# Kernel tuning notes

Hardware: AMD Instinct MI355X
Metric: run time of the kernel (lower is better)

## Reference

```python
import jax, jax.numpy as jnp
import numpy as np

H = 512; V = 100; V1 = V + 1; T = 20; L = 2; B = 1024; M = 5; K = 10; DFF = 4 * H
NEG = -1e9


def _ln(x, g, b):
    m = x.mean(-1, keepdims=True)
    v = x.var(-1, keepdims=True)
    return (x - m) / jnp.sqrt(v + 1e-5) * g + b


def _attn(q_in, kv_in, iw, ib, ow, ob, mask):
    # single-head attention, inputs [T,B,H] / [S,B,H]
    q = q_in @ iw[:H].T + ib[:H]
    k = kv_in @ iw[H:2 * H].T + ib[H:2 * H]
    v = kv_in @ iw[2 * H:].T + ib[2 * H:]
    s = jnp.einsum('qbh,kbh->bqk', q, k) / jnp.sqrt(jnp.float32(H))
    if mask is not None:
        s = s + mask
    a = jax.nn.softmax(s, axis=-1)
    o = jnp.einsum('bqk,kbh->qbh', a, v)
    return o @ ow.T + ob


def _pos_encoding(max_len, d):
    pos = jnp.arange(max_len, dtype=jnp.float32)[:, None]
    div = jnp.exp(jnp.arange(0, d, 2, dtype=jnp.float32) * (-np.log(10000.0) / d))
    pe = jnp.zeros((max_len, d), jnp.float32)
    pe = pe.at[:, 0::2].set(jnp.sin(pos * div)).at[:, 1::2].set(jnp.cos(pos * div))
    return pe[:, None, :]  # [T,1,H]


def setup_inputs() -> dict:
    key = jax.random.key(0)
    ks = jax.random.split(key, 20)
    s = 0.05
    rn = lambda k, shape: jax.random.normal(k, shape, jnp.float32) * s
    return dict(
        meanings=jax.random.randint(ks[0], (B, M), 0, K),
        emb_table=rn(ks[1], (M * K, H)),
        v2e_w=rn(ks[2], (H, V1)), v2e_b=rn(ks[3], (H,)),
        e2v_w=rn(ks[4], (V1, H)), e2v_b=rn(ks[5], (V1,)),
        sa_in_w=rn(ks[6], (L, 3 * H, H)), sa_in_b=rn(ks[7], (L, 3 * H)),
        sa_out_w=rn(ks[8], (L, H, H)), sa_out_b=rn(ks[9], (L, H)),
        ca_in_w=rn(ks[10], (L, 3 * H, H)), ca_in_b=rn(ks[11], (L, 3 * H)),
        ca_out_w=rn(ks[12], (L, H, H)), ca_out_b=rn(ks[13], (L, H)),
        ff1_w=rn(ks[14], (L, DFF, H)), ff1_b=rn(ks[15], (L, DFF)),
        ff2_w=rn(ks[16], (L, H, DFF)), ff2_b=rn(ks[17], (L, H)),
        ln_g=jnp.ones((L, 3, H), jnp.float32),
        ln_b=jnp.zeros((L, 3, H), jnp.float32),
    )


def reference(meanings, emb_table, v2e_w, v2e_b, e2v_w, e2v_b,
              sa_in_w, sa_in_b, sa_out_w, sa_out_b,
              ca_in_w, ca_in_b, ca_out_w, ca_out_b,
              ff1_w, ff1_b, ff2_w, ff2_b, ln_g, ln_b):
    bsz = meanings.shape[0]
    # meanings_offset = (cumsum(ones)-1)*K == arange(M)*K
    idx = meanings + jnp.arange(M) * K          # [B,M]
    src = emb_table[idx].sum(axis=1)[None]      # [1,B,H] memory
    pe = _pos_encoding(T, H)
    # start token one-hot probabilities
    probs = jnp.zeros((1, bsz, V1), jnp.float32).at[:, :, V].set(1.0)
    outs = []
    for i in range(T):
        x = probs @ v2e_w.T + v2e_b + pe[:i + 1]            # [i+1,B,H]
        mask = jnp.triu(jnp.full((i + 1, i + 1), NEG, jnp.float32), k=1)
        for l in range(L):
            x = _ln(x + _attn(x, x, sa_in_w[l], sa_in_b[l], sa_out_w[l], sa_out_b[l], mask),
                    ln_g[l, 0], ln_b[l, 0])
            x = _ln(x + _attn(x, src, ca_in_w[l], ca_in_b[l], ca_out_w[l], ca_out_b[l], None),
                    ln_g[l, 1], ln_b[l, 1])
            ff = jax.nn.relu(x @ ff1_w[l].T + ff1_b[l]) @ ff2_w[l].T + ff2_b[l]
            x = _ln(x + ff, ln_g[l, 2], ln_b[l, 2])
        logits = x @ e2v_w.T + e2v_b                        # [i+1,B,V1]
        last = logits[-1]                                   # [B,V1]
        outs.append(last)
        probs = jnp.concatenate([probs, jax.nn.softmax(last, axis=-1)[None]], axis=0)
    return jnp.stack(outs, axis=0)                          # [T,B,V1]
```

## Files before the change

### kernel.cpp

```cpp
#include <hip/hip_runtime.h>
#include <hip/hip_bf16.h>
#include <math.h>

#define Hdim 512
#define Vv   100
#define V1n  101
#define Tt   20
#define Ln   2
#define Bb   1024
#define Mm   5
#define Kk   10
#define DFFn 2048

typedef _Float16 f16;
typedef __attribute__((ext_vector_type(8))) _Float16 f16x8;
typedef __attribute__((ext_vector_type(16))) float f32x16;

static const size_t BH  = (size_t)Bb * Hdim;
static const size_t PSP = (size_t)Bb * 128;

__device__ __forceinline__ void split2(float v, f16* s) {
    f16 h0 = (f16)v;
    float r = v - (float)h0;
    s[0] = h0; s[1] = (f16)r;
}
__device__ __forceinline__ void xsp_write(f16* __restrict__ xsp, int row, int h, float v)
{
    f16 s[2]; split2(v, s);
    size_t o = (size_t)(h >> 3) * 8192 + (size_t)row * 8 + (h & 7);
    xsp[o] = s[0]; xsp[BH + o] = s[1];
}

template<int EPI>
__global__ __launch_bounds__(256, 2) void gemm_sp(
    const f16* __restrict__ Asp, const f16* __restrict__ Wsp,
    const float* __restrict__ bias,
    float* __restrict__ C, f16* __restrict__ Csp, size_t cplane,
    int N, int Kd, int kcount, int posn)
{
    __shared__ f16 lds[16384];
    const int tid = threadIdx.x;
    const int lane = tid & 63, w = tid >> 6;
    const int wm = w >> 1, wn = w & 1;
    const int bm = blockIdx.y * 128, bn = blockIdx.x * 128;
    const int kc0 = blockIdx.z * (kcount >> 3);
    const int nt = kcount >> 5;
    const int K8 = Kd >> 3;

    size_t gA[4], gB[4]; int lA[4], lB[4];
#pragma unroll
    for (int q = 0; q < 4; ++q) {
        int cid = q * 256 + tid, slab = cid >> 7, win = cid & 127;
        int p = slab >> 2, kcr = slab & 3;
        gA[q] = ((size_t)p * K8 + kc0 + kcr) * 8192 + (size_t)bm * 8 + win * 8;
        lA[q] = slab * 1024 + win * 8;
        gB[q] = ((size_t)p * K8 + kc0 + kcr) * ((size_t)N * 8) + (size_t)bn * 8 + win * 8;
        lB[q] = 8192 + slab * 1024 + win * 8;
    }

    f32x16 acc[2][2];
#pragma unroll
    for (int mi = 0; mi < 2; ++mi)
#pragma unroll
        for (int ni = 0; ni < 2; ++ni)
#pragma unroll
            for (int j = 0; j < 16; ++j) acc[mi][ni][j] = 0.f;

    f16x8 rA[4], rB[4];
#pragma unroll
    for (int q = 0; q < 4; ++q) {
        rA[q] = *(const f16x8*)(Asp + gA[q]);
        rB[q] = *(const f16x8*)(Wsp + gB[q]);
    }

    for (int t = 0; t < nt; ++t) {
        __syncthreads();
#pragma unroll
        for (int q = 0; q < 4; ++q) {
            *(f16x8*)&lds[lA[q]] = rA[q];
            *(f16x8*)&lds[lB[q]] = rB[q];
        }
        __syncthreads();
        if (t + 1 < nt) {
#pragma unroll
            for (int q = 0; q < 4; ++q) {
                rA[q] = *(const f16x8*)(Asp + gA[q] + (size_t)(t + 1) * 32768);
                rB[q] = *(const f16x8*)(Wsp + gB[q] + (size_t)(t + 1) * 32 * N);
            }
        }
#pragma unroll
        for (int ks = 0; ks < 2; ++ks) {
            const int kb = (2 * ks + (lane >> 5)) * 1024 + (lane & 31) * 8;
            f16x8 a[2][2], b[2][2];
#pragma unroll
            for (int mi = 0; mi < 2; ++mi)
#pragma unroll
                for (int p = 0; p < 2; ++p)
                    a[mi][p] = *(const f16x8*)&lds[p * 4096 + kb + (64 * wm + 32 * mi) * 8];
#pragma unroll
            for (int ni = 0; ni < 2; ++ni)
#pragma unroll
                for (int p = 0; p < 2; ++p)
                    b[ni][p] = *(const f16x8*)&lds[8192 + p * 4096 + kb + (64 * wn + 32 * ni) * 8];
#pragma unroll
            for (int mi = 0; mi < 2; ++mi)
#pragma unroll
                for (int ni = 0; ni < 2; ++ni) {
                    f32x16 v = acc[mi][ni];
                    v = __builtin_amdgcn_mfma_f32_32x32x16_f16(a[mi][1], b[ni][0], v, 0, 0, 0);
                    v = __builtin_amdgcn_mfma_f32_32x32x16_f16(a[mi][0], b[ni][1], v, 0, 0, 0);
                    v = __builtin_amdgcn_mfma_f32_32x32x16_f16(a[mi][0], b[ni][0], v, 0, 0, 0);
                    acc[mi][ni] = v;
                }
        }
    }

    const int er0 = bm + 64 * wm + 4 * (lane >> 5);
    const int ec0 = bn + 64 * wn + (lane & 31);
#pragma unroll
    for (int mi = 0; mi < 2; ++mi) {
#pragma unroll
        for (int ni = 0; ni < 2; ++ni) {
            int col = ec0 + 32 * ni;
#pragma unroll
            for (int r = 0; r < 16; ++r) {
                int row = er0 + 32 * mi + (r & 3) + 8 * (r >> 2);
                float v = acc[mi][ni][r];
                if (EPI == 0) {
                    C[(size_t)blockIdx.z * Bb * N + (size_t)row * N + col] = v;
                } else if (EPI == 1) {
                    v = fmaxf(v + bias[col], 0.f);
                    f16 s[2]; split2(v, s);
                    size_t o = (size_t)(col >> 3) * 8192 + (size_t)row * 8 + (col & 7);
                    Csp[o] = s[0]; Csp[cplane + o] = s[1];
                } else if (EPI == 3) {
                    v += bias[col];
                    f16 s[2]; split2(v, s);
                    size_t o = (size_t)(col >> 3) * 8192 + (size_t)row * 8 + (col & 7);
                    Csp[o] = s[0]; Csp[cplane + o] = s[1];
                } else if (EPI == 4) {
                    C[(size_t)row * N + col] = v + bias[col];
                } else if (EPI == 5) {
                    v += bias[col];
                    int j2 = col & ~1;
                    float div = expf(-(float)j2 * (logf(10000.f) / (float)Hdim));
                    float ang = (float)posn * div;
                    v += (col & 1) ? cosf(ang) : sinf(ang);
                    C[(size_t)row * Hdim + col] = v;
                    f16 s[2]; split2(v, s);
                    size_t o = (size_t)(col >> 3) * 8192 + (size_t)row * 8 + (col & 7);
                    Csp[o] = s[0]; Csp[cplane + o] = s[1];
                }
            }
        }
    }
}

__global__ void split_mat(const float* __restrict__ src, f16* __restrict__ dst,
                          int Nreal, int Npad, int Kreal, int kpl)
{
    int i = blockIdx.x * 256 + threadIdx.x;
    int Kpad = 1 << kpl;
    if (i >= (Npad << kpl)) return;
    int n = i >> kpl, k = i & (Kpad - 1);
    float v = (n < Nreal && k < Kreal) ? src[(size_t)n * Kreal + k] : 0.f;
    f16 s[2]; split2(v, s);
    size_t plane = (size_t)Npad << kpl;
    size_t o = (size_t)(k >> 3) * ((size_t)Npad * 8) + (size_t)n * 8 + (k & 7);
    dst[o] = s[0]; dst[plane + o] = s[1];
}

__global__ void src_kernel(const int* __restrict__ meanings,
                           const float* __restrict__ emb, f16* __restrict__ ssp)
{
    int idx = blockIdx.x * 256 + threadIdx.x;
    int b = idx >> 9, h = idx & 511;
    float s = 0.f;
#pragma unroll
    for (int m = 0; m < Mm; ++m) {
        int row = meanings[b * Mm + m] + m * Kk;
        s += emb[(size_t)row * Hdim + h];
    }
    xsp_write(ssp, b, h, s);
}

__global__ void init_x(const float* __restrict__ v2e_w, const float* __restrict__ v2e_b,
                       float* __restrict__ x, f16* __restrict__ xsp)
{
    int idx = blockIdx.x * 256 + threadIdx.x;
    int b = idx >> 9, h = idx & 511;
    float s = v2e_w[(size_t)h * V1n + Vv] + v2e_b[h] + ((h & 1) ? 1.f : 0.f);
    x[idx] = s;
    xsp_write(xsp, b, h, s);
}

__global__ __launch_bounds__(256) void attn_fused(
    const float* __restrict__ P, const float* __restrict__ bias3h,
    float* __restrict__ kc, float* __restrict__ vc,
    f16* __restrict__ osplit, int step)
{
    __shared__ float qs[Hdim];
    __shared__ float ssm[32];
    __shared__ float wts[32];
    int b = blockIdx.x, tid = threadIdx.x, lane = tid & 63, wv = tid >> 6;
    const size_t PS = (size_t)Bb * 1536;
    const float* pb = P + (size_t)b * 1536;
#pragma unroll
    for (int c0 = 0; c0 < 2; ++c0) {
        int c = tid + c0 * 256;
        float qv = bias3h[c]        + pb[c]        + pb[PS + c];
        float kv = bias3h[512 + c]  + pb[512 + c]  + pb[PS + 512 + c];
        float vv = bias3h[1024 + c] + pb[1024 + c] + pb[PS + 1024 + c];
        qs[c] = qv;
        kc[((size_t)step * Bb + b) * Hdim + c] = kv;
        vc[((size_t)step * Bb + b) * Hdim + c] = vv;
    }
    __syncthreads();
    const float4* q4 = (const float4*)qs;
    for (int t = wv; t <= step; t += 4) {
        const float4* k4 = (const float4*)(kc + ((size_t)t * Bb + b) * Hdim);
        float4 qa = q4[lane], ka = k4[lane];
        float4 qb = q4[lane + 64], kb = k4[lane + 64];
        float p = qa.x*ka.x + qa.y*ka.y + qa.z*ka.z + qa.w*ka.w
                + qb.x*kb.x + qb.y*kb.y + qb.z*kb.z + qb.w*kb.w;
#pragma unroll
        for (int off = 32; off; off >>= 1) p += __shfl_down(p, off);
        if (!lane) ssm[t] = p * 0.044194173824159216f;
    }
    __syncthreads();
    float m = -1e30f;
    for (int t = 0; t <= step; ++t) m = fmaxf(m, ssm[t]);
    float den = 0.f;
    for (int t = 0; t <= step; ++t) den += expf(ssm[t] - m);
    if (tid <= step) wts[tid] = expf(ssm[tid] - m) / den;
    __syncthreads();
#pragma unroll
    for (int c0 = 0; c0 < 2; ++c0) {
        int h = tid + c0 * 256;
        float a2 = 0.f;
        for (int t = 0; t <= step; ++t)
            a2 += wts[t] * vc[((size_t)t * Bb + b) * Hdim + h];
        xsp_write(osplit, b, h, a2);
    }
}

__device__ __forceinline__ float2 rowstats(float v0, float v1, float* sh)
{
    __syncthreads();
    float s = v0 + v1, s2 = v0 * v0 + v1 * v1;
    int lane = threadIdx.x & 63, wv = threadIdx.x >> 6;
#pragma unroll
    for (int off = 32; off; off >>= 1) {
        s += __shfl_down(s, off);
        s2 += __shfl_down(s2, off);
    }
    if (!lane) { sh[wv] = s; sh[wv + 4] = s2; }
    __syncthreads();
    float S = sh[0] + sh[1] + sh[2] + sh[3];
    float S2 = sh[4] + sh[5] + sh[6] + sh[7];
    float mean = S * (1.f / Hdim);
    float var = S2 * (1.f / Hdim) - mean * mean;
    return make_float2(mean, rsqrtf(var + 1e-5f));
}

template<int NZ>
__global__ __launch_bounds__(256) void ln12(
    float* __restrict__ x, const float* __restrict__ P, const float* __restrict__ ob,
    const float* __restrict__ cross,
    const float* __restrict__ g0, const float* __restrict__ b0,
    const float* __restrict__ g1, const float* __restrict__ b1,
    f16* __restrict__ xsp)
{
    __shared__ float sh[8];
    size_t base = (size_t)blockIdx.x * Hdim;
    int tid = threadIdx.x;
    float v0 = x[base + tid] + ob[tid];
    float v1 = x[base + tid + 256] + ob[tid + 256];
#pragma unroll
    for (int z = 0; z < NZ; ++z) {
        v0 += P[z * BH + base + tid];
        v1 += P[z * BH + base + tid + 256];
    }
    float2 st = rowstats(v0, v1, sh);
    float y0 = (v0 - st.x) * st.y * g0[tid] + b0[tid] + cross[base + tid];
    float y1 = (v1 - st.x) * st.y * g0[tid + 256] + b0[tid + 256] + cross[base + tid + 256];
    float2 s2 = rowstats(y0, y1, sh);
    float o0 = (y0 - s2.x) * s2.y * g1[tid] + b1[tid];
    float o1 = (y1 - s2.x) * s2.y * g1[tid + 256] + b1[tid + 256];
    x[base + tid] = o0; x[base + tid + 256] = o1;
    xsp_write(xsp, blockIdx.x, tid, o0);
    xsp_write(xsp, blockIdx.x, tid + 256, o1);
}

template<int NZ>
__global__ __launch_bounds__(256) void ln3(
    float* __restrict__ x, const float* __restrict__ P, const float* __restrict__ fb,
    const float* __restrict__ g, const float* __restrict__ bbv, f16* __restrict__ xsp)
{
    __shared__ float sh[8];
    size_t base = (size_t)blockIdx.x * Hdim;
    int tid = threadIdx.x;
    float v0 = x[base + tid] + fb[tid];
    float v1 = x[base + tid + 256] + fb[tid + 256];
#pragma unroll
    for (int z = 0; z < NZ; ++z) {
        v0 += P[z * BH + base + tid];
        v1 += P[z * BH + base + tid + 256];
    }
    float2 st = rowstats(v0, v1, sh);
    float o0 = (v0 - st.x) * st.y * g[tid] + bbv[tid];
    float o1 = (v1 - st.x) * st.y * g[tid + 256] + bbv[tid + 256];
    x[base + tid] = o0; x[base + tid + 256] = o1;
    xsp_write(xsp, blockIdx.x, tid, o0);
    xsp_write(xsp, blockIdx.x, tid + 256, o1);
}

__global__ __launch_bounds__(128) void softmax_out(
    const float* __restrict__ P, const float* __restrict__ e2v_b,
    float* __restrict__ out_i, f16* __restrict__ psp)
{
    __shared__ float red[4];
    int b = blockIdx.x, v = threadIdx.x, lane = v & 63, wv = v >> 6;
    bool valid = v < V1n;
    float s = -1e30f;
    if (valid) {
        s = e2v_b[v];
#pragma unroll
        for (int z = 0; z < 4; ++z) s += P[(size_t)z * Bb * 128 + (size_t)b * 128 + v];
        out_i[(size_t)b * V1n + v] = s;
    }
    float m = s;
#pragma unroll
    for (int off = 32; off; off >>= 1) m = fmaxf(m, __shfl_xor(m, off));
    if (!lane) red[wv] = m;
    __syncthreads();
    float M = fmaxf(red[0], red[1]);
    float e = valid ? expf(s - M) : 0.f;
    float d = e;
#pragma unroll
    for (int off = 32; off; off >>= 1) d += __shfl_xor(d, off);
    if (!lane) red[2 + wv] = d;
    __syncthreads();
    float D = red[2] + red[3];
    float p = valid ? e / D : 0.f;
    f16 t2[2]; split2(p, t2);
    size_t o = (size_t)(v >> 3) * 8192 + (size_t)b * 8 + (v & 7);
    psp[o] = t2[0]; psp[PSP + o] = t2[1];
}

extern "C" void kernel_launch(void* const* d_in, const int* in_sizes, int n_in,
                              void* d_out, int out_size, void* d_ws, size_t ws_size,
                              hipStream_t stream)
{
    const int*   meanings = (const int*)  d_in[0];
    const float* emb      = (const float*)d_in[1];
    const float* v2e_w    = (const float*)d_in[2];
    const float* v2e_b    = (const float*)d_in[3];
    const float* e2v_w    = (const float*)d_in[4];
    const float* e2v_b    = (const float*)d_in[5];
    const float* sa_in_w  = (const float*)d_in[6];
    const float* sa_in_b  = (const float*)d_in[7];
    const float* sa_out_w = (const float*)d_in[8];
    const float* sa_out_b = (const float*)d_in[9];
    const float* ca_in_w  = (const float*)d_in[10];
    const float* ca_in_b  = (const float*)d_in[11];
    const float* ca_out_w = (const float*)d_in[12];
    const float* ca_out_b = (const float*)d_in[13];
    const float* ff1_w    = (const float*)d_in[14];
    const float* ff1_b    = (const float*)d_in[15];
    const float* ff2_w    = (const float*)d_in[16];
    const float* ff2_b    = (const float*)d_in[17];
    const float* ln_g     = (const float*)d_in[18];
    const float* ln_b     = (const float*)d_in[19];
    float* out = (float*)d_out;

    char* wsb = (char*)d_ws;
    auto alloc = [&](size_t bytes) {
        char* p = wsb; wsb += (bytes + 255) & ~(size_t)255; return p;
    };
    const int nsain = 1536 * 512, nsaout = 512 * 512, nff1 = 2048 * 512,
              nff2 = 512 * 2048, nca = 512 * 512;
    f16 *wsp_sa_in[2], *wsp_sa_out[2], *wsp_ff1[2], *wsp_ff2[2];
    for (int l = 0; l < 2; ++l) wsp_sa_in[l]  = (f16*)alloc((size_t)2 * nsain * 2);
    for (int l = 0; l < 2; ++l) wsp_sa_out[l] = (f16*)alloc((size_t)2 * nsaout * 2);
    for (int l = 0; l < 2; ++l) wsp_ff1[l]    = (f16*)alloc((size_t)2 * nff1 * 2);
    for (int l = 0; l < 2; ++l) wsp_ff2[l]    = (f16*)alloc((size_t)2 * nff2 * 2);
    float* x       = (float*)alloc(BH * 4);
    f16*   xsp     = (f16*)  alloc(2 * BH * 2);
    float* cross   = (float*)alloc(2 * BH * 4);
    float* Pbuf    = (float*)alloc(8 * BH * 4);
    f16*   h1sp    = (f16*)  alloc(2 * (size_t)Bb * DFFn * 2);
    f16*   psp     = (f16*)  alloc(2 * PSP * 2);
    f16*   e2v_wsp = (f16*)  alloc((size_t)2 * 128 * 512 * 2);
    f16*   v2e_wsp = (f16*)  alloc((size_t)2 * 512 * 128 * 2);
    float* kc      = (float*)alloc((size_t)Ln * Tt * BH * 4);
    float* vc      = (float*)alloc((size_t)Ln * Tt * BH * 4);
    f16* ssp    = h1sp;
    f16* wspc_v = (f16*)Pbuf;
    f16* wspc_o = wspc_v + (size_t)2 * nca;
    f16* vssp   = wspc_o + (size_t)2 * nca;

    const float* srcs[8] = { sa_in_w, sa_in_w + nsain, sa_out_w, sa_out_w + nsaout,
                             ff1_w, ff1_w + nff1, ff2_w, ff2_w + nff2 };
    f16* dsts[8] = { wsp_sa_in[0], wsp_sa_in[1], wsp_sa_out[0], wsp_sa_out[1],
                     wsp_ff1[0], wsp_ff1[1], wsp_ff2[0], wsp_ff2[1] };
    int nN[8] = { 1536, 1536, 512, 512, 2048, 2048, 512, 512 };
    int kb[8] = { 9, 9, 9, 9, 9, 9, 11, 11 };
    for (int i = 0; i < 8; ++i)
        split_mat<<<(nN[i] << kb[i]) / 256, 256, 0, stream>>>(
            srcs[i], dsts[i], nN[i], nN[i], 1 << kb[i], kb[i]);
    split_mat<<<(128 << 9) / 256, 256, 0, stream>>>(e2v_w, e2v_wsp, V1n, 128, 512, 9);
    split_mat<<<(512 << 7) / 256, 256, 0, stream>>>(v2e_w, v2e_wsp, 512, 512, V1n, 7);

    src_kernel<<<BH / 256, 256, 0, stream>>>(meanings, emb, ssp);
    for (int l = 0; l < Ln; ++l) {
        split_mat<<<nca / 256, 256, 0, stream>>>(
            ca_in_w + (size_t)l * 3 * Hdim * Hdim + (size_t)2 * Hdim * Hdim,
            wspc_v, 512, 512, 512, 9);
        split_mat<<<nca / 256, 256, 0, stream>>>(
            ca_out_w + (size_t)l * Hdim * Hdim, wspc_o, 512, 512, 512, 9);
        gemm_sp<3><<<dim3(4, 8, 1), 256, 0, stream>>>(
            ssp, wspc_v, ca_in_b + l * 1536 + 1024,
            nullptr, vssp, BH, 512, 512, 512, 0);
        gemm_sp<4><<<dim3(4, 8, 1), 256, 0, stream>>>(
            vssp, wspc_o, ca_out_b + l * 512,
            cross + (size_t)l * BH, nullptr, 0, 512, 512, 512, 0);
    }
    init_x<<<BH / 256, 256, 0, stream>>>(v2e_w, v2e_b, x, xsp);

    for (int i = 0; i < Tt; ++i) {
        for (int l = 0; l < Ln; ++l) {
            float* kcl = kc + (size_t)l * Tt * BH;
            float* vcl = vc + (size_t)l * Tt * BH;
            gemm_sp<0><<<dim3(12, 8, 2), 256, 0, stream>>>(
                xsp, wsp_sa_in[l], nullptr,
                Pbuf, nullptr, 0, 1536, 512, 256, 0);
            attn_fused<<<Bb, 256, 0, stream>>>(Pbuf, sa_in_b + l * 1536,
                                               kcl, vcl, xsp, i);
            gemm_sp<0><<<dim3(4, 8, 8), 256, 0, stream>>>(
                xsp, wsp_sa_out[l], nullptr,
                Pbuf, nullptr, 0, 512, 512, 64, 0);
            ln12<8><<<Bb, 256, 0, stream>>>(x, Pbuf, sa_out_b + l * 512,
                cross + (size_t)l * BH,
                ln_g + (size_t)(l * 3 + 0) * Hdim, ln_b + (size_t)(l * 3 + 0) * Hdim,
                ln_g + (size_t)(l * 3 + 1) * Hdim, ln_b + (size_t)(l * 3 + 1) * Hdim,
                xsp);
            gemm_sp<1><<<dim3(16, 8, 1), 256, 0, stream>>>(
                xsp, wsp_ff1[l], ff1_b + l * 2048,
                nullptr, h1sp, (size_t)Bb * DFFn, 2048, 512, 512, 0);
            gemm_sp<0><<<dim3(4, 8, 8), 256, 0, stream>>>(
                h1sp, wsp_ff2[l], nullptr,
                Pbuf, nullptr, 0, 512, 2048, 256, 0);
            ln3<8><<<Bb, 256, 0, stream>>>(x, Pbuf, ff2_b + l * 512,
                ln_g + (size_t)(l * 3 + 2) * Hdim, ln_b + (size_t)(l * 3 + 2) * Hdim,
                xsp);
        }
        gemm_sp<0><<<dim3(1, 8, 4), 256, 0, stream>>>(
            xsp, e2v_wsp, nullptr, Pbuf, nullptr, 0, 128, 512, 128, 0);
        softmax_out<<<Bb, 128, 0, stream>>>(
            Pbuf, e2v_b, out + (size_t)i * Bb * V1n, psp);
        if (i + 1 < Tt)
            gemm_sp<5><<<dim3(4, 8, 1), 256, 0, stream>>>(
                psp, v2e_wsp, v2e_b, x, xsp, BH, 512, 128, 128, i + 1);
    }
}
```

Before: 3.727 ms.

## Double GEMM K-tile depth and split FF1 along K with separate combine

The split-fp16 MFMA GEMM now stages 64 K-elements per iteration instead of 32. This doubles LDS use and prefetch registers but halves the number of barrier and load rounds. FF1 no longer applies bias, ReLU and the split in its epilogue. It runs as a 2-way split-K GEMM into fp32 partials, and a new vectorised combine kernel sums them, applies bias and ReLU, and writes the split fp16 layout. This doubles the block count for the 128-block FF1 launch on a many-CU GPU, at the cost of an extra round trip of fp32 partials through memory and one more launch. The LN kernels drop their unused template parameter.

```diff
diff --git a/kernel.cpp b/kernel.cpp
--- a/kernel.cpp
+++ b/kernel.cpp
@@ -38,24 +38,24 @@
     float* __restrict__ C, f16* __restrict__ Csp, size_t cplane,
     int N, int Kd, int kcount, int posn)
 {
-    __shared__ f16 lds[16384];
+    __shared__ f16 lds[32768];
     const int tid = threadIdx.x;
     const int lane = tid & 63, w = tid >> 6;
     const int wm = w >> 1, wn = w & 1;
     const int bm = blockIdx.y * 128, bn = blockIdx.x * 128;
     const int kc0 = blockIdx.z * (kcount >> 3);
-    const int nt = kcount >> 5;
+    const int nt = kcount >> 6;
     const int K8 = Kd >> 3;
 
-    size_t gA[4], gB[4]; int lA[4], lB[4];
-#pragma unroll
-    for (int q = 0; q < 4; ++q) {
+    size_t gA[8], gB[8]; int lA[8], lB[8];
+#pragma unroll
+    for (int q = 0; q < 8; ++q) {
         int cid = q * 256 + tid, slab = cid >> 7, win = cid & 127;
-        int p = slab >> 2, kcr = slab & 3;
+        int p = slab >> 3, kcr = slab & 7;
         gA[q] = ((size_t)p * K8 + kc0 + kcr) * 8192 + (size_t)bm * 8 + win * 8;
         lA[q] = slab * 1024 + win * 8;
         gB[q] = ((size_t)p * K8 + kc0 + kcr) * ((size_t)N * 8) + (size_t)bn * 8 + win * 8;
-        lB[q] = 8192 + slab * 1024 + win * 8;
+        lB[q] = 16384 + slab * 1024 + win * 8;
     }
 
     f32x16 acc[2][2];
@@ -66,9 +66,9 @@
 #pragma unroll
             for (int j = 0; j < 16; ++j) acc[mi][ni][j] = 0.f;
 
-    f16x8 rA[4], rB[4];
-#pragma unroll
-    for (int q = 0; q < 4; ++q) {
+    f16x8 rA[8], rB[8];
+#pragma unroll
+    for (int q = 0; q < 8; ++q) {
         rA[q] = *(const f16x8*)(Asp + gA[q]);
         rB[q] = *(const f16x8*)(Wsp + gB[q]);
     }
@@ -76,32 +76,32 @@
     for (int t = 0; t < nt; ++t) {
         __syncthreads();
 #pragma unroll
-        for (int q = 0; q < 4; ++q) {
+        for (int q = 0; q < 8; ++q) {
             *(f16x8*)&lds[lA[q]] = rA[q];
             *(f16x8*)&lds[lB[q]] = rB[q];
         }
         __syncthreads();
         if (t + 1 < nt) {
 #pragma unroll
-            for (int q = 0; q < 4; ++q) {
-                rA[q] = *(const f16x8*)(Asp + gA[q] + (size_t)(t + 1) * 32768);
-                rB[q] = *(const f16x8*)(Wsp + gB[q] + (size_t)(t + 1) * 32 * N);
+            for (int q = 0; q < 8; ++q) {
+                rA[q] = *(const f16x8*)(Asp + gA[q] + (size_t)(t + 1) * 65536);
+                rB[q] = *(const f16x8*)(Wsp + gB[q] + (size_t)(t + 1) * 64 * N);
             }
         }
 #pragma unroll
-        for (int ks = 0; ks < 2; ++ks) {
+        for (int ks = 0; ks < 4; ++ks) {
             const int kb = (2 * ks + (lane >> 5)) * 1024 + (lane & 31) * 8;
             f16x8 a[2][2], b[2][2];
 #pragma unroll
             for (int mi = 0; mi < 2; ++mi)
 #pragma unroll
                 for (int p = 0; p < 2; ++p)
-                    a[mi][p] = *(const f16x8*)&lds[p * 4096 + kb + (64 * wm + 32 * mi) * 8];
+                    a[mi][p] = *(const f16x8*)&lds[p * 8192 + kb + (64 * wm + 32 * mi) * 8];
 #pragma unroll
             for (int ni = 0; ni < 2; ++ni)
 #pragma unroll
                 for (int p = 0; p < 2; ++p)
-                    b[ni][p] = *(const f16x8*)&lds[8192 + p * 4096 + kb + (64 * wn + 32 * ni) * 8];
+                    b[ni][p] = *(const f16x8*)&lds[16384 + p * 8192 + kb + (64 * wn + 32 * ni) * 8];
 #pragma unroll
             for (int mi = 0; mi < 2; ++mi)
 #pragma unroll
@@ -128,11 +128,6 @@
                 float v = acc[mi][ni][r];
                 if (EPI == 0) {
                     C[(size_t)blockIdx.z * Bb * N + (size_t)row * N + col] = v;
-                } else if (EPI == 1) {
-                    v = fmaxf(v + bias[col], 0.f);
-                    f16 s[2]; split2(v, s);
-                    size_t o = (size_t)(col >> 3) * 8192 + (size_t)row * 8 + (col & 7);
-                    Csp[o] = s[0]; Csp[cplane + o] = s[1];
                 } else if (EPI == 3) {
                     v += bias[col];
                     f16 s[2]; split2(v, s);
@@ -156,6 +151,26 @@
     }
 }
 
+__global__ __launch_bounds__(256) void ff1_combine(
+    const float* __restrict__ P, const float* __restrict__ bias,
+    f16* __restrict__ hsp)
+{
+    const size_t PS = (size_t)Bb * DFFn;
+    size_t base = ((size_t)blockIdx.x * 256 + threadIdx.x) * 4;
+    int row = (int)(base >> 11), col = (int)(base & (DFFn - 1));
+    float4 bv = *(const float4*)(bias + col);
+    float4 p0 = *(const float4*)(P + base);
+    float4 p1 = *(const float4*)(P + PS + base);
+    float vv[4] = { fmaxf(bv.x + p0.x + p1.x, 0.f), fmaxf(bv.y + p0.y + p1.y, 0.f),
+                    fmaxf(bv.z + p0.z + p1.z, 0.f), fmaxf(bv.w + p0.w + p1.w, 0.f) };
+    size_t o = (size_t)(col >> 3) * 8192 + (size_t)row * 8 + (col & 7);
+#pragma unroll
+    for (int j = 0; j < 4; ++j) {
+        f16 s[2]; split2(vv[j], s);
+        hsp[o + j] = s[0]; hsp[PS + o + j] = s[1];
+    }
+}
+
 __global__ void split_mat(const float* __restrict__ src, f16* __restrict__ dst,
                           int Nreal, int Npad, int Kreal, int kpl)
 {
@@ -263,7 +278,6 @@
     return make_float2(mean, rsqrtf(var + 1e-5f));
 }
 
-template<int NZ>
 __global__ __launch_bounds__(256) void ln12(
     float* __restrict__ x, const float* __restrict__ P, const float* __restrict__ ob,
     const float* __restrict__ cross,
@@ -277,7 +291,7 @@
     float v0 = x[base + tid] + ob[tid];
     float v1 = x[base + tid + 256] + ob[tid + 256];
 #pragma unroll
-    for (int z = 0; z < NZ; ++z) {
+    for (int z = 0; z < 8; ++z) {
         v0 += P[z * BH + base + tid];
         v1 += P[z * BH + base + tid + 256];
     }
@@ -292,7 +306,6 @@
     xsp_write(xsp, blockIdx.x, tid + 256, o1);
 }
 
-template<int NZ>
 __global__ __launch_bounds__(256) void ln3(
     float* __restrict__ x, const float* __restrict__ P, const float* __restrict__ fb,
     const float* __restrict__ g, const float* __restrict__ bbv, f16* __restrict__ xsp)
@@ -303,7 +316,7 @@
     float v0 = x[base + tid] + fb[tid];
     float v1 = x[base + tid + 256] + fb[tid + 256];
 #pragma unroll
-    for (int z = 0; z < NZ; ++z) {
+    for (int z = 0; z < 8; ++z) {
         v0 += P[z * BH + base + tid];
         v1 += P[z * BH + base + tid + 256];
     }
@@ -440,18 +453,20 @@
             gemm_sp<0><<<dim3(4, 8, 8), 256, 0, stream>>>(
                 xsp, wsp_sa_out[l], nullptr,
                 Pbuf, nullptr, 0, 512, 512, 64, 0);
-            ln12<8><<<Bb, 256, 0, stream>>>(x, Pbuf, sa_out_b + l * 512,
+            ln12<<<Bb, 256, 0, stream>>>(x, Pbuf, sa_out_b + l * 512,
                 cross + (size_t)l * BH,
                 ln_g + (size_t)(l * 3 + 0) * Hdim, ln_b + (size_t)(l * 3 + 0) * Hdim,
                 ln_g + (size_t)(l * 3 + 1) * Hdim, ln_b + (size_t)(l * 3 + 1) * Hdim,
                 xsp);
-            gemm_sp<1><<<dim3(16, 8, 1), 256, 0, stream>>>(
-                xsp, wsp_ff1[l], ff1_b + l * 2048,
-                nullptr, h1sp, (size_t)Bb * DFFn, 2048, 512, 512, 0);
+            gemm_sp<0><<<dim3(16, 8, 2), 256, 0, stream>>>(
+                xsp, wsp_ff1[l], nullptr,
+                Pbuf, nullptr, 0, 2048, 512, 256, 0);
+            ff1_combine<<<(Bb * DFFn / 4) / 256, 256, 0, stream>>>(
+                Pbuf, ff1_b + l * 2048, h1sp);
             gemm_sp<0><<<dim3(4, 8, 8), 256, 0, stream>>>(
                 h1sp, wsp_ff2[l], nullptr,
                 Pbuf, nullptr, 0, 512, 2048, 256, 0);
-            ln3<8><<<Bb, 256, 0, stream>>>(x, Pbuf, ff2_b + l * 512,
+            ln3<<<Bb, 256, 0, stream>>>(x, Pbuf, ff2_b + l * 512,
                 ln_g + (size_t)(l * 3 + 2) * Hdim, ln_b + (size_t)(l * 3 + 2) * Hdim,
                 xsp);
         }
```

Measured after the change: 4.096 ms. 1.1x slower.
